# Kernel optimization log

Measured on AMD Instinct MI355X. Metric: run time of the kernel, lower is better.

The kernel has to match this reference:

```python
import jax, jax.numpy as jnp
import numpy as np

B, C, CO, N = 2, 32, 32, 64
MODES, LMAX, RBINS = 16, 2, 16
HALF = MODES // 2
NL = (LMAX + 1) ** 2  # 9 real spherical harmonics up to l=2
M = MODES ** 3
HID = 16  # round(CO * 0.5)


def _build_basis():
    # frequencies of the kept FNO corner modes along each axis
    f = np.concatenate([np.arange(HALF), np.arange(-HALF, 0)]).astype(np.float32)
    kx, ky, kz = np.meshgrid(f, f, f, indexing='ij')
    kx, ky, kz = kx.ravel(), ky.ravel(), kz.ravel()
    r = np.sqrt(kx ** 2 + ky ** 2 + kz ** 2)
    nzm = (r > 0).astype(np.float32)
    inv = np.where(r > 0, 1.0 / np.maximum(r, 1e-9), 0.0)
    ux, uy, uz = kx * inv, ky * inv, kz * inv
    # real spherical harmonics l=0,1,2 (cartesian form); all l>0 vanish at DC
    Y = np.stack([
        0.282095 * np.ones_like(r),
        0.488603 * uy, 0.488603 * uz, 0.488603 * ux,
        1.092548 * ux * uy, 1.092548 * uy * uz,
        0.315392 * (3.0 * uz ** 2 - nzm),
        1.092548 * ux * uz, 0.546274 * (ux ** 2 - uy ** 2)], axis=0)  # [NL, M]
    shell = np.minimum((r / (r.max() + 1e-6) * RBINS).astype(np.int64), RBINS - 1)
    cnt = np.bincount(shell, minlength=RBINS).astype(np.float32)
    w = 1.0 / np.sqrt(np.maximum(cnt, 1.0))
    mask = (shell[None, :] == np.arange(RBINS)[:, None]).astype(np.float32) * w[:, None]  # [RBINS, M]
    return (mask[:, None, :] * Y[None]).reshape(RBINS * NL, M).astype(np.float32)

BASIS = jnp.asarray(_build_basis())  # [K=144, M=4096], fixed projection basis
IDX = jnp.asarray(np.concatenate([np.arange(HALF), np.arange(N - HALF, N)]))  # kept mode indices


def cgelu(z):
    return jax.nn.gelu(z.real) + 1j * jax.nn.gelu(z.imag)


def setup_inputs() -> dict:
    key = jax.random.key(0)
    ks = jax.random.split(key, 17)
    rn = lambda k, s: jax.random.normal(k, s, dtype=jnp.float32)
    return {
        'x': rn(ks[0], (B, C, N, N, N)),
        'w_fno_r': rn(ks[1], (CO, C)) * 0.1, 'w_fno_i': rn(ks[2], (CO, C)) * 0.1,
        'b_fno_r': rn(ks[3], (CO,)) * 0.1, 'b_fno_i': rn(ks[4], (CO,)) * 0.1,
        'w_gate_r': rn(ks[5], (CO,)), 'w_gate_i': rn(ks[6], (CO,)),
        'w_spec_r': rn(ks[7], (RBINS, NL, C, CO)) * 0.1, 'w_spec_i': rn(ks[8], (RBINS, NL, C, CO)) * 0.1,
        'mlp_w1_r': rn(ks[9], (HID, CO)) * 0.1, 'mlp_w1_i': rn(ks[10], (HID, CO)) * 0.1,
        'mlp_b1_r': rn(ks[11], (HID,)) * 0.1, 'mlp_b1_i': rn(ks[12], (HID,)) * 0.1,
        'mlp_w2_r': rn(ks[13], (CO, HID)) * 0.1, 'mlp_w2_i': rn(ks[14], (CO, HID)) * 0.1,
        'mlp_b2_r': rn(ks[15], (CO,)) * 0.1, 'mlp_b2_i': rn(ks[16], (CO,)) * 0.1,
    }


def reference(x, w_fno_r, w_fno_i, b_fno_r, b_fno_i, w_gate_r, w_gate_i,
              w_spec_r, w_spec_i, mlp_w1_r, mlp_w1_i, mlp_b1_r, mlp_b1_i,
              mlp_w2_r, mlp_w2_i, mlp_b2_r, mlp_b2_i):
    cx = lambda r, i: (r + 1j * i).astype(jnp.complex64)
    xc = x.astype(jnp.complex64)
    w_fno, b_fno = cx(w_fno_r, w_fno_i), cx(b_fno_r, b_fno_i)
    w_gate = cx(w_gate_r, w_gate_i)
    w_spec = cx(w_spec_r, w_spec_i)
    w1, b1 = cx(mlp_w1_r, mlp_w1_i), cx(mlp_b1_r, mlp_b1_i)
    w2, b2 = cx(mlp_w2_r, mlp_w2_i), cx(mlp_b2_r, mlp_b2_i)

    # skip paths: complex 1x1-conv ('linear') and complex soft-gating
    skip_fno = jnp.einsum('oc,bcxyz->boxyz', w_fno, xc) + b_fno[None, :, None, None, None]
    skip_mlp = xc * w_gate[None, :, None, None, None]

    # Harmonic layer: FFT -> slice kept modes -> harmonic/radial projection
    # -> complex spectral conv -> inverse projection -> scatter -> iFFT
    xf = jnp.fft.fftn(xc, axes=(-3, -2, -1))
    xs = xf[:, :, IDX[:, None, None], IDX[None, :, None], IDX[None, None, :]].reshape(B, C, M)
    coeffs = jnp.einsum('bcm,km->bck', xs, BASIS).reshape(B, C, RBINS, NL)
    coeffs = jnp.einsum('bisl,slio->bosl', coeffs, w_spec)
    xs2 = jnp.einsum('bck,km->bcm', coeffs.reshape(B, CO, RBINS * NL), BASIS)
    full = jnp.zeros((B, CO, N, N, N), jnp.complex64).at[
        :, :, IDX[:, None, None], IDX[None, :, None], IDX[None, None, :]
    ].set(xs2.reshape(B, CO, MODES, MODES, MODES))
    x_fno = jnp.fft.ifftn(full, axes=(-3, -2, -1))

    x1 = x_fno + skip_fno  # n_layers=1 -> no activation here
    h = cgelu(jnp.einsum('hc,bcxyz->bhxyz', w1, x1) + b1[None, :, None, None, None])
    y = jnp.einsum('oh,bhxyz->boxyz', w2, h) + b2[None, :, None, None, None]
    return (y + skip_mlp).real
```

## Files before the change

kernel.cpp:

```cpp
#include <hip/hip_runtime.h>
#include <hip/hip_bf16.h>

#define PI2 6.283185307179586f

typedef __attribute__((ext_vector_type(8))) short short8;
typedef __attribute__((ext_vector_type(4))) float f32x4;

static const size_t O_Y      = 0;
static const size_t O_W1RT   = 36864;
static const size_t O_W1IT   = 37376;
static const size_t O_W1XR   = 37888;
static const size_t O_W1XI   = 38400;
static const size_t O_B1PR   = 38912;
static const size_t O_B1PI   = 38928;
static const size_t O_WSH    = 38944;
static const size_t O_SHELL  = 38960;
static const size_t O_ORDER  = 43056;
static const size_t O_SSTART = 47152;
static const size_t O_COEF   = 47232;
static const size_t O_COEF2  = 65664;
static const size_t O_XS     = 84096;
static const size_t O_XS2    = 608384;
static const size_t O_T2     = 1132672;
static const size_t O_T1     = 3229824;

static __device__ __forceinline__ float geluf(float v) {
  float u = 0.7978845608028654f * (v + 0.044715f * v * v * v);
  float a = fabsf(u);
  float e = __expf(-2.0f * a);
  float th = (1.0f - e) / (1.0f + e);
  th = copysignf(th, u);
  return 0.5f * v * (1.0f + th);
}

static __device__ __forceinline__ unsigned int f2bfbits(float f) {
  unsigned int u = __float_as_uint(f);
  u += 0x7fffu + ((u >> 16) & 1u);
  return u >> 16;
}

static __device__ __forceinline__ unsigned int pk2(float a, float b) {
  return f2bfbits(a) | (f2bfbits(b) << 16);
}

__global__ __launch_bounds__(256) void k0_init(
    const float* __restrict__ wfr, const float* __restrict__ wfi,
    const float* __restrict__ bfr, const float* __restrict__ bfi,
    const float* __restrict__ w1r, const float* __restrict__ w1i,
    const float* __restrict__ b1r, const float* __restrict__ b1i,
    float* __restrict__ ws) {
  float* Y    = ws + O_Y;
  float* w1rt = ws + O_W1RT;  float* w1it = ws + O_W1IT;
  float* W1xr = ws + O_W1XR;  float* W1xi = ws + O_W1XI;
  float* b1pr = ws + O_B1PR;  float* b1pi = ws + O_B1PI;
  float* wsh  = ws + O_WSH;
  int* shellOf = (int*)(ws + O_SHELL);
  int* order   = (int*)(ws + O_ORDER);
  int* sstart  = (int*)(ws + O_SSTART);

  __shared__ int cnt[16], fill[16], st[17];
  int tid = threadIdx.x;
  if (tid < 16) { cnt[tid] = 0; fill[tid] = 0; }
  __syncthreads();
  for (int m = tid; m < 4096; m += 256) {
    int ix = m >> 8, iy = (m >> 4) & 15, iz = m & 15;
    float kx = (float)(ix < 8 ? ix : ix - 16);
    float ky = (float)(iy < 8 ? iy : iy - 16);
    float kz = (float)(iz < 8 ? iz : iz - 16);
    float r2 = kx*kx + ky*ky + kz*kz;
    float r  = sqrtf(r2);
    float nzm = r2 > 0.f ? 1.f : 0.f;
    float inv = r2 > 0.f ? 1.0f / fmaxf(r, 1e-9f) : 0.f;
    float ux = kx*inv, uy = ky*inv, uz = kz*inv;
    Y[0*4096+m] = 0.282095f;
    Y[1*4096+m] = 0.488603f * uy;
    Y[2*4096+m] = 0.488603f * uz;
    Y[3*4096+m] = 0.488603f * ux;
    Y[4*4096+m] = 1.092548f * ux*uy;
    Y[5*4096+m] = 1.092548f * uy*uz;
    Y[6*4096+m] = 0.315392f * (3.0f*uz*uz - nzm);
    Y[7*4096+m] = 1.092548f * ux*uz;
    Y[8*4096+m] = 0.546274f * (ux*ux - uy*uy);
    float rmax = sqrtf(192.0f);
    float t = r / (rmax + 1e-6f) * 16.0f;
    int sh = (int)t; sh = sh > 15 ? 15 : sh;
    shellOf[m] = sh;
    atomicAdd(&cnt[sh], 1);
  }
  __syncthreads();
  if (tid == 0) { int a = 0; for (int s = 0; s < 16; ++s) { st[s] = a; a += cnt[s]; } st[16] = a; }
  __syncthreads();
  if (tid < 16) wsh[tid] = 1.0f / sqrtf(fmaxf((float)cnt[tid], 1.0f));
  if (tid < 17) sstart[tid] = st[tid];
  for (int m = tid; m < 4096; m += 256) {
    int sh = shellOf[m];
    int p = atomicAdd(&fill[sh], 1);
    order[st[sh] + p] = m;
  }
  for (int e = tid; e < 512; e += 256) {
    int j = e >> 5, c = e & 31;
    float ar = 0.f, ai = 0.f;
    for (int o = 0; o < 32; ++o) {
      float wr_ = w1r[j*32+o], wi_ = w1i[j*32+o];
      float fr  = wfr[o*32+c], fi_ = wfi[o*32+c];
      ar += wr_*fr - wi_*fi_;
      ai += wr_*fi_ + wi_*fr;
    }
    W1xr[c*16+j] = ar;  W1xi[c*16+j] = ai;
    w1rt[c*16+j] = w1r[j*32+c];
    w1it[c*16+j] = w1i[j*32+c];
  }
  if (tid < 16) {
    int j = tid;
    float ar = b1r[j], ai = b1i[j];
    for (int o = 0; o < 32; ++o) {
      ar += w1r[j*32+o]*bfr[o] - w1i[j*32+o]*bfi[o];
      ai += w1r[j*32+o]*bfi[o] + w1i[j*32+o]*bfr[o];
    }
    b1pr[j] = ar; b1pi[j] = ai;
  }
}

__global__ __launch_bounds__(256) void k12_fwd(const float* __restrict__ x, float* __restrict__ T2) {
  __shared__ float plane[64*68];
  __shared__ float2 slab[64*17];
  float* ysum = plane;
  float2* tw2 = (float2*)(plane + 2592);
  int blk = blockIdx.x;
  const float* src = x + (size_t)blk * 4096;
  int tid = threadIdx.x;
  for (int i = tid; i < 4096; i += 256) {
    int y = i >> 6, z = i & 63;
    plane[z*68 + y] = src[i];
  }
  __syncthreads();
  {
    int kz = tid & 15, yq = tid >> 4;
    float f = (float)(kz < 8 ? kz : kz - 16);
    float ang = -PI2 * f / 64.0f;
    float sw, cw; __sincosf(ang, &sw, &cw);
    float tr = 1.f, ti = 0.f;
    float a0r=0,a0i=0,a1r=0,a1i=0,a2r=0,a2i=0,a3r=0,a3i=0;
    for (int z = 0; z < 64; ++z) {
      float4 xv = *(const float4*)&plane[z*68 + 4*yq];
      a0r += xv.x*tr; a0i += xv.x*ti;
      a1r += xv.y*tr; a1i += xv.y*ti;
      a2r += xv.z*tr; a2i += xv.z*ti;
      a3r += xv.w*tr; a3i += xv.w*ti;
      float nt = tr*cw - ti*sw; ti = tr*sw + ti*cw; tr = nt;
    }
    int y0 = 4*yq;
    slab[(y0+0)*17 + kz] = make_float2(a0r, a0i);
    slab[(y0+1)*17 + kz] = make_float2(a1r, a1i);
    slab[(y0+2)*17 + kz] = make_float2(a2r, a2i);
    slab[(y0+3)*17 + kz] = make_float2(a3r, a3i);
  }
  __syncthreads();
  {
    int k = tid >> 4, i2 = tid & 15;
    float f = (float)(k < 8 ? k : k - 16);
    float ang = -PI2 * f * (float)i2 / 64.0f;
    float sw, cw; __sincosf(ang, &sw, &cw);
    tw2[k*17 + i2] = make_float2(cw, sw);
  }
  {
    int y0 = tid >> 4, kz = tid & 15;
    float2 u0 = slab[(y0     )*17 + kz];
    float2 u1 = slab[(y0 + 16)*17 + kz];
    float2 u2 = slab[(y0 + 32)*17 + kz];
    float2 u3 = slab[(y0 + 48)*17 + kz];
    float Ar = u0.x + u2.x, Ai = u0.y + u2.y;
    float Br = u0.x - u2.x, Bi = u0.y - u2.y;
    float Cr = u1.x + u3.x, Ci = u1.y + u3.y;
    float Dr = u1.x - u3.x, Di = u1.y - u3.y;
    float* yp = ysum + y0*162 + kz*10;
    yp[0] = Ar + Cr;  yp[1] = Ai + Ci;
    yp[2] = Br + Di;  yp[3] = Bi - Dr;
    yp[4] = Ar - Cr;  yp[5] = Ai - Ci;
    yp[6] = Br - Di;  yp[7] = Bi + Dr;
  }
  __syncthreads();
  {
    int kz = tid & 15, kyi = tid >> 4;
    const float* yp = ysum + kz*10 + (kyi & 3)*2;
    const float2* twp = tw2 + kyi*17;
    float ar = 0.f, ai = 0.f;
    #pragma unroll
    for (int y0 = 0; y0 < 16; ++y0) {
      float sr = yp[y0*162], si = yp[y0*162 + 1];
      float2 tw = twp[y0];
      ar += sr*tw.x - si*tw.y;
      ai += sr*tw.y + si*tw.x;
    }
    *(float2*)&T2[(size_t)blk*512 + (kyi*16 + kz)*2] = make_float2(ar, ai);
  }
}

__global__ __launch_bounds__(256) void k3_dftx(const float* __restrict__ T2, float* __restrict__ xs) {
  __shared__ float slab[64*34];
  __shared__ float xsum[2592];
  __shared__ float2 twx[16*17];
  int blk = blockIdx.x;
  int bc = blk >> 4, ky = blk & 15;
  int tid = threadIdx.x;
  for (int i = tid; i < 2048; i += 256) {
    int xr = i >> 5, rem = i & 31;
    slab[xr*34 + rem] = T2[((size_t)(bc*64 + xr)*16 + ky)*32 + rem];
  }
  {
    int k = tid >> 4, i2 = tid & 15;
    float f = (float)(k < 8 ? k : k - 16);
    float ang = -PI2 * f * (float)i2 / 64.0f;
    float sw, cw; __sincosf(ang, &sw, &cw);
    twx[k*17 + i2] = make_float2(cw, sw);
  }
  __syncthreads();
  {
    int x0 = tid >> 4, kz = tid & 15;
    const float2* sp = (const float2*)slab;
    float2 u0 = sp[(x0     )*17 + kz];
    float2 u1 = sp[(x0 + 16)*17 + kz];
    float2 u2 = sp[(x0 + 32)*17 + kz];
    float2 u3 = sp[(x0 + 48)*17 + kz];
    float Ar = u0.x + u2.x, Ai = u0.y + u2.y;
    float Br = u0.x - u2.x, Bi = u0.y - u2.y;
    float Cr = u1.x + u3.x, Ci = u1.y + u3.y;
    float Dr = u1.x - u3.x, Di = u1.y - u3.y;
    float* yp = xsum + x0*162 + kz*10;
    yp[0] = Ar + Cr;  yp[1] = Ai + Ci;
    yp[2] = Br + Di;  yp[3] = Bi - Dr;
    yp[4] = Ar - Cr;  yp[5] = Ai - Ci;
    yp[6] = Br - Di;  yp[7] = Bi + Dr;
  }
  __syncthreads();
  {
    int kz = tid & 15, kxi = tid >> 4;
    const float* yp = xsum + kz*10 + (kxi & 3)*2;
    const float2* twp = twx + kxi*17;
    float ar = 0.f, ai = 0.f;
    #pragma unroll
    for (int x0 = 0; x0 < 16; ++x0) {
      float sr = yp[x0*162], si = yp[x0*162 + 1];
      float2 tw = twp[x0];
      ar += sr*tw.x - si*tw.y;
      ai += sr*tw.y + si*tw.x;
    }
    *(float2*)&xs[(size_t)bc*8192 + (kxi*256 + ky*16 + kz)*2] = make_float2(ar, ai);
  }
}

__global__ __launch_bounds__(256) void k4_proj(const float* __restrict__ xs, const float* __restrict__ Y,
    const int* __restrict__ order, const int* __restrict__ sstart, const float* __restrict__ wsh,
    float* __restrict__ coeffs) {
  int blk = blockIdx.x; int bc = blk >> 4, s = blk & 15;
  int tid = threadIdx.x;
  int st = sstart[s], en = sstart[s+1];
  float ar[9], ai[9];
  #pragma unroll
  for (int l = 0; l < 9; ++l) { ar[l] = 0.f; ai[l] = 0.f; }
  for (int ii = st + tid; ii < en; ii += 256) {
    int m = order[ii];
    float2 v = *(const float2*)&xs[(size_t)bc*8192 + m*2];
    #pragma unroll
    for (int l = 0; l < 9; ++l) {
      float yv = Y[l*4096 + m];
      ar[l] += yv * v.x; ai[l] += yv * v.y;
    }
  }
  __shared__ float red[256*19];
  #pragma unroll
  for (int l = 0; l < 9; ++l) { red[tid*19 + l] = ar[l]; red[tid*19 + 9 + l] = ai[l]; }
  __syncthreads();
  for (int r = 128; r >= 1; r >>= 1) {
    if (tid < r) {
      #pragma unroll
      for (int q = 0; q < 18; ++q) red[tid*19 + q] += red[(tid + r)*19 + q];
    }
    __syncthreads();
  }
  if (tid == 0) {
    float w = wsh[s];
    for (int l = 0; l < 9; ++l) {
      coeffs[((size_t)bc*144 + s*9 + l)*2]     = w * red[l];
      coeffs[((size_t)bc*144 + s*9 + l)*2 + 1] = w * red[9 + l];
    }
  }
}

__global__ __launch_bounds__(64) void k5_spec(const float* __restrict__ coeffs,
    const float* __restrict__ wsr, const float* __restrict__ wsi, float* __restrict__ coeffs2) {
  int blk = blockIdx.x;
  int b = blk / 144, sl = blk % 144;
  int o = threadIdx.x;
  if (o >= 32) return;
  float ar = 0.f, ai = 0.f;
  for (int i = 0; i < 32; ++i) {
    float cr = coeffs[((size_t)(b*32 + i)*144 + sl)*2];
    float ci = coeffs[((size_t)(b*32 + i)*144 + sl)*2 + 1];
    float wr = wsr[(sl*32 + i)*32 + o];
    float wi = wsi[(sl*32 + i)*32 + o];
    ar += cr*wr - ci*wi;
    ai += cr*wi + ci*wr;
  }
  const float sc = 1.0f / 262144.0f;
  coeffs2[((size_t)(b*32 + o)*144 + sl)*2]     = ar * sc;
  coeffs2[((size_t)(b*32 + o)*144 + sl)*2 + 1] = ai * sc;
}

__global__ __launch_bounds__(256) void k7_unproj(const float* __restrict__ coeffs2, const float* __restrict__ Y,
    const int* __restrict__ shellOf, const float* __restrict__ wsh, float* __restrict__ xs2) {
  int bo = blockIdx.x >> 4;
  int m = ((blockIdx.x & 15) << 8) | threadIdx.x;
  __shared__ float c2[288];
  for (int i = threadIdx.x; i < 288; i += 256) c2[i] = coeffs2[(size_t)bo*288 + i];
  __syncthreads();
  int sh = shellOf[m];
  float w = wsh[sh];
  float ar = 0.f, ai = 0.f;
  #pragma unroll
  for (int l = 0; l < 9; ++l) {
    float yv = Y[l*4096 + m];
    ar += yv * c2[(sh*9 + l)*2];
    ai += yv * c2[(sh*9 + l)*2 + 1];
  }
  xs2[(size_t)bo*8192 + m*2]     = w * ar;
  xs2[(size_t)bo*8192 + m*2 + 1] = w * ai;
}

__global__ __launch_bounds__(256) void k8_invx(const float* __restrict__ xs2, float* __restrict__ U1) {
  __shared__ float slab[512];
  int blk = blockIdx.x;
  int bo = blk >> 4, ky = blk & 15;
  int tid = threadIdx.x;
  for (int i = tid; i < 512; i += 256) {
    int kx = i >> 5, rem = i & 31;
    slab[i] = xs2[(size_t)bo*8192 + kx*512 + ky*32 + rem];
  }
  __syncthreads();
  int kz = tid & 15, grp = tid >> 4;
  float ang = PI2 * (float)grp / 64.0f;
  float sw, cw; __sincosf(ang, &sw, &cw);
  float tr = 1.f, ti = 0.f;
  float sjr[4] = {0.f,0.f,0.f,0.f}, sji[4] = {0.f,0.f,0.f,0.f};
  #pragma unroll
  for (int kx = 0; kx < 16; ++kx) {
    if (kx == 8) ti = -ti;
    float2 v = *(const float2*)&slab[(kx*16 + kz)*2];
    sjr[kx & 3] += v.x*tr - v.y*ti;
    sji[kx & 3] += v.x*ti + v.y*tr;
    float nt = tr*cw - ti*sw; ti = tr*sw + ti*cw; tr = nt;
  }
  float Ar = sjr[0]+sjr[2], Ai = sji[0]+sji[2];
  float Br = sjr[0]-sjr[2], Bi = sji[0]-sji[2];
  float Cr = sjr[1]+sjr[3], Ci = sji[1]+sji[3];
  float Dr = sjr[1]-sjr[3], Di = sji[1]-sji[3];
  *(float2*)&U1[((size_t)(bo*64 + grp     )*16 + ky)*32 + kz*2] = make_float2(Ar+Cr, Ai+Ci);
  *(float2*)&U1[((size_t)(bo*64 + grp + 16)*16 + ky)*32 + kz*2] = make_float2(Br-Di, Bi+Dr);
  *(float2*)&U1[((size_t)(bo*64 + grp + 32)*16 + ky)*32 + kz*2] = make_float2(Ar-Cr, Ai-Ci);
  *(float2*)&U1[((size_t)(bo*64 + grp + 48)*16 + ky)*32 + kz*2] = make_float2(Br+Di, Bi-Dr);
}

__global__ __launch_bounds__(256) void k9_invy(const float* __restrict__ U1, float* __restrict__ U2) {
  __shared__ float slab[512];
  int blk = blockIdx.x;
  int tid = threadIdx.x;
  const float* src = U1 + (size_t)blk * 512;
  for (int i = tid; i < 512; i += 256) slab[i] = src[i];
  __syncthreads();
  int kz = tid & 15, grp = tid >> 4;
  float ang = PI2 * (float)grp / 64.0f;
  float sw, cw; __sincosf(ang, &sw, &cw);
  float tr = 1.f, ti = 0.f;
  float sjr[4] = {0.f,0.f,0.f,0.f}, sji[4] = {0.f,0.f,0.f,0.f};
  #pragma unroll
  for (int ky = 0; ky < 16; ++ky) {
    if (ky == 8) ti = -ti;
    float2 v = *(const float2*)&slab[(ky*16 + kz)*2];
    sjr[ky & 3] += v.x*tr - v.y*ti;
    sji[ky & 3] += v.x*ti + v.y*tr;
    float nt = tr*cw - ti*sw; ti = tr*sw + ti*cw; tr = nt;
  }
  float Ar = sjr[0]+sjr[2], Ai = sji[0]+sji[2];
  float Br = sjr[0]-sjr[2], Bi = sji[0]-sji[2];
  float Cr = sjr[1]+sjr[3], Ci = sji[1]+sji[3];
  float Dr = sjr[1]-sjr[3], Di = sji[1]-sji[3];
  float* dst = U2 + (size_t)blk * 2048;
  *(float2*)&dst[((grp     )*16 + kz)*2] = make_float2(Ar+Cr, Ai+Ci);
  *(float2*)&dst[((grp + 16)*16 + kz)*2] = make_float2(Br-Di, Bi+Dr);
  *(float2*)&dst[((grp + 32)*16 + kz)*2] = make_float2(Ar-Cr, Ai-Ci);
  *(float2*)&dst[((grp + 48)*16 + kz)*2] = make_float2(Br+Di, Bi-Dr);
}

__global__ __launch_bounds__(256) void k10_final(
    const float* __restrict__ x, const float* __restrict__ U2,
    const float* __restrict__ ws,
    const float* __restrict__ w2r, const float* __restrict__ w2i,
    const float* __restrict__ b2r, const float* __restrict__ wgr,
    float* __restrict__ out) {
  const float* w1rt = ws + O_W1RT;  const float* w1it = ws + O_W1IT;
  const float* W1xr = ws + O_W1XR;  const float* W1xi = ws + O_W1XI;
  const float* b1pr = ws + O_B1PR;  const float* b1pi = ws + O_B1PI;

  __shared__ unsigned int xfT[128*33];
  __shared__ __hip_bfloat16 xlT[128*34];
  __shared__ unsigned int hpW[4*272];
  float* scratch = (float*)xfT;
  float2* twz = (float2*)hpW;

  int tid = threadIdx.x;
  int blk = blockIdx.x;
  int yb = blk & 31, bx = blk >> 5;
  int b = bx >> 6, xr = bx & 63;
  int y0 = yb * 2;

  for (int i = tid; i < 1024; i += 256) {
    int ya = i >> 9, c = (i >> 4) & 31, zq = i & 15;
    const float4 v = *(const float4*)&x[(size_t)(b*32 + c)*262144 + (size_t)xr*4096
                                        + (size_t)(y0 + ya)*64 + 4*zq];
    int rb = ((ya << 6) + 4*zq)*34 + c;
    xlT[rb]       = __float2bfloat16(v.x);
    xlT[rb + 34]  = __float2bfloat16(v.y);
    xlT[rb + 68]  = __float2bfloat16(v.z);
    xlT[rb + 102] = __float2bfloat16(v.w);
  }
  for (int e = tid; e < 1024; e += 256) {
    int q = e & 15, o = (e >> 4) & 31, ya = e >> 9;
    const float2* g = (const float2*)(U2 + ((size_t)((b*32 + o)*64 + xr))*2048 + (size_t)(y0 + ya)*32);
    *(float2*)&scratch[(ya*32 + o)*34 + 2*q] = g[q];
  }
  {
    int k = tid >> 4, i2 = tid & 15;
    float f = (float)(k < 8 ? k : k - 16);
    float ang = PI2 * f * (float)i2 / 64.0f;
    float sw, cw; __sincosf(ang, &sw, &cw);
    twz[k*17 + i2] = make_float2(cw, sw);
  }
  __syncthreads();

  {
    int o = tid & 31, r3 = tid >> 5;
    int ya = r3 >> 2, zq = r3 & 3;
    float ur[16], ui[16];
    const float2* sp = (const float2*)&scratch[(ya*32 + o)*34];
    #pragma unroll
    for (int q = 0; q < 16; ++q) { float2 v = sp[q]; ur[q] = v.x; ui[q] = v.y; }
    __syncthreads();

    #pragma unroll
    for (int t = 0; t < 4; ++t) {
      int z0 = 4*zq + t;
      float sr[4] = {0.f, 0.f, 0.f, 0.f}, si[4] = {0.f, 0.f, 0.f, 0.f};
      #pragma unroll
      for (int k = 0; k < 16; ++k) {
        float2 tw = twz[k*17 + z0];
        sr[k & 3] += ur[k]*tw.x - ui[k]*tw.y;
        si[k & 3] += ur[k]*tw.y + ui[k]*tw.x;
      }
      float Ar = sr[0]+sr[2], Ai = si[0]+si[2];
      float Br = sr[0]-sr[2], Bi = si[0]-si[2];
      float Cr = sr[1]+sr[3], Ci = si[1]+si[3];
      float Dr = sr[1]-sr[3], Di = si[1]-si[3];
      int rb = (ya << 6) + z0;
      xfT[rb*33 + o]        = pk2(Ar+Cr, Ai+Ci);
      xfT[(rb+16)*33 + o]   = pk2(Br-Di, Bi+Dr);
      xfT[(rb+32)*33 + o]   = pk2(Ar-Cr, Ai-Ci);
      xfT[(rb+48)*33 + o]   = pk2(Br+Di, Bi-Dr);
    }
  }
  __syncthreads();

  {
    int lane = tid & 63, wv = tid >> 6;
    int p = lane & 15, q = lane >> 4;
    int wb = wv * 272;

    union U8 { short8 v; unsigned int u[4]; };
    U8 fW1r, fW1i, fW1iN, fW1xr, fW1xi, fW2[2];
    #pragma unroll
    for (int s = 0; s < 4; ++s) {
      int c0 = 8*q + 2*s, c1 = c0 + 1;
      fW1r.u[s]  = pk2(w1rt[c0*16 + p], w1rt[c1*16 + p]);
      fW1i.u[s]  = pk2(w1it[c0*16 + p], w1it[c1*16 + p]);
      fW1iN.u[s] = fW1i.u[s] ^ 0x80008000u;
      fW1xr.u[s] = pk2(W1xr[c0*16 + p], W1xr[c1*16 + p]);
      fW1xi.u[s] = pk2(W1xi[c0*16 + p], W1xi[c1*16 + p]);
    }
    #pragma unroll
    for (int mt = 0; mt < 2; ++mt) {
      int o = mt*16 + p;
      #pragma unroll
      for (int s = 0; s < 4; ++s) {
        int k0 = 8*q + 2*s;
        float a  = (k0   < 16) ? w2r[o*16 + k0]      : -w2i[o*16 + k0 - 16];
        float bb = (k0+1 < 16) ? w2r[o*16 + k0 + 1]  : -w2i[o*16 + k0 - 15];
        fW2[mt].u[s] = pk2(a, bb);
      }
    }
    float4 b1r4 = *(const float4*)(b1pr + 4*q);
    float4 b1i4 = *(const float4*)(b1pi + 4*q);
    float b2a[2][4], wga[2][4];
    #pragma unroll
    for (int mt = 0; mt < 2; ++mt) {
      float4 t0 = *(const float4*)(b2r + mt*16 + 4*q);
      float4 t1 = *(const float4*)(wgr + mt*16 + 4*q);
      b2a[mt][0]=t0.x; b2a[mt][1]=t0.y; b2a[mt][2]=t0.z; b2a[mt][3]=t0.w;
      wga[mt][0]=t1.x; wga[mt][1]=t1.y; wga[mt][2]=t1.z; wga[mt][3]=t1.w;
    }
    float b1ra[4] = {b1r4.x, b1r4.y, b1r4.z, b1r4.w};
    float b1ia[4] = {b1i4.x, b1i4.y, b1i4.z, b1i4.w};

    f32x4 zacc = {0.f, 0.f, 0.f, 0.f};
    const unsigned int* xlW = (const unsigned int*)xlT;

    for (int tt = 0; tt < 2; ++tt) {
      int tile = wv*2 + tt;
      int ya = tile >> 2, zg = tile & 3;
      int row = ya*64 + zg*16 + p;

      unsigned int w8[8];
      #pragma unroll
      for (int jj = 0; jj < 8; ++jj) w8[jj] = xfT[row*33 + 8*q + jj];
      U8 FR, FI, XV;
      #pragma unroll
      for (int s = 0; s < 4; ++s) {
        FR.u[s] = __builtin_amdgcn_perm(w8[2*s+1], w8[2*s], 0x05040100u);
        FI.u[s] = __builtin_amdgcn_perm(w8[2*s+1], w8[2*s], 0x07060302u);
        XV.u[s] = xlW[row*17 + 4*q + s];
      }

      f32x4 accR = zacc, accI = zacc;
      accR = __builtin_amdgcn_mfma_f32_16x16x32_bf16(fW1r.v,  FR.v, accR, 0, 0, 0);
      accR = __builtin_amdgcn_mfma_f32_16x16x32_bf16(fW1iN.v, FI.v, accR, 0, 0, 0);
      accR = __builtin_amdgcn_mfma_f32_16x16x32_bf16(fW1xr.v, XV.v, accR, 0, 0, 0);
      accI = __builtin_amdgcn_mfma_f32_16x16x32_bf16(fW1r.v,  FI.v, accI, 0, 0, 0);
      accI = __builtin_amdgcn_mfma_f32_16x16x32_bf16(fW1i.v,  FR.v, accI, 0, 0, 0);
      accI = __builtin_amdgcn_mfma_f32_16x16x32_bf16(fW1xi.v, XV.v, accI, 0, 0, 0);

      float hr_[4], hi_[4];
      #pragma unroll
      for (int r = 0; r < 4; ++r) {
        hr_[r] = geluf(accR[r] + b1ra[r]);
        hi_[r] = geluf(accI[r] + b1ia[r]);
      }
      hpW[wb + 17*p + 2*q]     = pk2(hr_[0], hr_[1]);
      hpW[wb + 17*p + 2*q + 1] = pk2(hr_[2], hr_[3]);
      hpW[wb + 17*p + 8 + 2*q]     = pk2(hi_[0], hi_[1]);
      hpW[wb + 17*p + 8 + 2*q + 1] = pk2(hi_[2], hi_[3]);

      U8 FH;
      #pragma unroll
      for (int s = 0; s < 4; ++s) FH.u[s] = hpW[wb + 17*p + 4*q + s];

      #pragma unroll
      for (int mt = 0; mt < 2; ++mt) {
        f32x4 accO = __builtin_amdgcn_mfma_f32_16x16x32_bf16(fW2[mt].v, FH.v, zacc, 0, 0, 0);
        #pragma unroll
        for (int r = 0; r < 4; ++r) {
          int o = mt*16 + q*4 + r;
          int z = zg*16 + p;
          float xv = __bfloat162float(xlT[row*34 + o]);
          out[(size_t)(b*32 + o)*262144 + (size_t)xr*4096 + (size_t)(y0 + ya)*64 + z]
              = accO[r] + b2a[mt][r] + wga[mt][r]*xv;
        }
      }
    }
  }
}

extern "C" void kernel_launch(void* const* d_in, const int* in_sizes, int n_in,
                              void* d_out, int out_size, void* d_ws, size_t ws_size,
                              hipStream_t stream) {
  (void)in_sizes; (void)n_in; (void)out_size; (void)ws_size;
  const float* x   = (const float*)d_in[0];
  const float* wfr = (const float*)d_in[1];
  const float* wfi = (const float*)d_in[2];
  const float* bfr = (const float*)d_in[3];
  const float* bfi = (const float*)d_in[4];
  const float* wgr = (const float*)d_in[5];
  const float* wsr = (const float*)d_in[7];
  const float* wsi = (const float*)d_in[8];
  const float* w1r = (const float*)d_in[9];
  const float* w1i = (const float*)d_in[10];
  const float* b1r = (const float*)d_in[11];
  const float* b1i = (const float*)d_in[12];
  const float* w2r = (const float*)d_in[13];
  const float* w2i = (const float*)d_in[14];
  const float* b2r = (const float*)d_in[15];
  float* out = (float*)d_out;
  float* ws  = (float*)d_ws;

  float* T1      = ws + O_T1;
  float* T2      = ws + O_T2;
  float* xs      = ws + O_XS;
  float* xs2     = ws + O_XS2;
  float* coeffs  = ws + O_COEF;
  float* coeffs2 = ws + O_COEF2;
  float* Y       = ws + O_Y;
  int* shellOf   = (int*)(ws + O_SHELL);
  int* order     = (int*)(ws + O_ORDER);
  int* sstart    = (int*)(ws + O_SSTART);
  float* wsh     = ws + O_WSH;

  hipLaunchKernelGGL(k0_init,  dim3(1),    dim3(256), 0, stream, wfr, wfi, bfr, bfi, w1r, w1i, b1r, b1i, ws);
  hipLaunchKernelGGL(k12_fwd,  dim3(4096), dim3(256), 0, stream, x, T2);
  hipLaunchKernelGGL(k3_dftx,  dim3(1024), dim3(256), 0, stream, T2, xs);
  hipLaunchKernelGGL(k4_proj,  dim3(1024), dim3(256), 0, stream, xs, Y, order, sstart, wsh, coeffs);
  hipLaunchKernelGGL(k5_spec,  dim3(288),  dim3(64),  0, stream, coeffs, wsr, wsi, coeffs2);
  hipLaunchKernelGGL(k7_unproj,dim3(1024), dim3(256), 0, stream, coeffs2, Y, shellOf, wsh, xs2);
  hipLaunchKernelGGL(k8_invx,  dim3(1024), dim3(256), 0, stream, xs2, T2);
  hipLaunchKernelGGL(k9_invy,  dim3(4096), dim3(256), 0, stream, T2, T1);
  hipLaunchKernelGGL(k10_final,dim3(4096), dim3(256), 0, stream, x, T1, ws, w2r, w2i, b2r, wgr, out);
}
```

Baseline: 273.9 us.

## Radix-4 pre-split z DFT in forward kernel and vectorize twiddle loads

```diff
diff --git a/kernel.cpp b/kernel.cpp
--- a/kernel.cpp
+++ b/kernel.cpp
@@ -122,47 +122,82 @@
 }
 
 __global__ __launch_bounds__(256) void k12_fwd(const float* __restrict__ x, float* __restrict__ T2) {
-  __shared__ float plane[64*68];
+  __shared__ __align__(16) float zS[4096];
   __shared__ float2 slab[64*17];
-  float* ysum = plane;
-  float2* tw2 = (float2*)(plane + 2592);
+  __shared__ float2 tw[16*17];
+  float* zP = zS;  float* zQ = zS + 1024;  float* zB = zS + 2048;  float* zD = zS + 3072;
+  float* ysum = zS;
   int blk = blockIdx.x;
   const float* src = x + (size_t)blk * 4096;
   int tid = threadIdx.x;
-  for (int i = tid; i < 4096; i += 256) {
-    int y = i >> 6, z = i & 63;
-    plane[z*68 + y] = src[i];
-  }
-  __syncthreads();
-  {
-    int kz = tid & 15, yq = tid >> 4;
-    float f = (float)(kz < 8 ? kz : kz - 16);
-    float ang = -PI2 * f / 64.0f;
-    float sw, cw; __sincosf(ang, &sw, &cw);
-    float tr = 1.f, ti = 0.f;
-    float a0r=0,a0i=0,a1r=0,a1i=0,a2r=0,a2i=0,a3r=0,a3i=0;
-    for (int z = 0; z < 64; ++z) {
-      float4 xv = *(const float4*)&plane[z*68 + 4*yq];
-      a0r += xv.x*tr; a0i += xv.x*ti;
-      a1r += xv.y*tr; a1i += xv.y*ti;
-      a2r += xv.z*tr; a2i += xv.z*ti;
-      a3r += xv.w*tr; a3i += xv.w*ti;
-      float nt = tr*cw - ti*sw; ti = tr*sw + ti*cw; tr = nt;
-    }
-    int y0 = 4*yq;
-    slab[(y0+0)*17 + kz] = make_float2(a0r, a0i);
-    slab[(y0+1)*17 + kz] = make_float2(a1r, a1i);
-    slab[(y0+2)*17 + kz] = make_float2(a2r, a2i);
-    slab[(y0+3)*17 + kz] = make_float2(a3r, a3i);
-  }
-  __syncthreads();
+
+  {
+    int y = tid >> 2, zt = tid & 3;
+    const float4* s4 = (const float4*)(src + y*64);
+    float4 u0 = s4[zt];
+    float4 u1 = s4[zt + 4];
+    float4 u2 = s4[zt + 8];
+    float4 u3 = s4[zt + 12];
+    const float* p0 = (const float*)&u0; const float* p1 = (const float*)&u1;
+    const float* p2 = (const float*)&u2; const float* p3 = (const float*)&u3;
+    int base = 4*zt*64 + y;
+    #pragma unroll
+    for (int e = 0; e < 4; ++e) {
+      float a = p0[e] + p2[e], c = p1[e] + p3[e];
+      float bb = p0[e] - p2[e], d = p1[e] - p3[e];
+      zP[base + e*64] = a + c;
+      zQ[base + e*64] = a - c;
+      zB[base + e*64] = bb;
+      zD[base + e*64] = d;
+    }
+  }
   {
     int k = tid >> 4, i2 = tid & 15;
     float f = (float)(k < 8 ? k : k - 16);
     float ang = -PI2 * f * (float)i2 / 64.0f;
     float sw, cw; __sincosf(ang, &sw, &cw);
-    tw2[k*17 + i2] = make_float2(cw, sw);
-  }
+    tw[k*17 + i2] = make_float2(cw, sw);
+  }
+  __syncthreads();
+
+  {
+    int kz = tid & 15, yq = tid >> 4;
+    int j = kz & 3;
+    const float2* twp = tw + kz*17;
+    float arr[4] = {0.f,0.f,0.f,0.f}, aii[4] = {0.f,0.f,0.f,0.f};
+    if ((j & 1) == 0) {
+      const float* plane = (j == 0) ? zP : zQ;
+      #pragma unroll
+      for (int z0 = 0; z0 < 16; ++z0) {
+        float2 w = twp[z0];
+        float4 s = *(const float4*)&plane[z0*64 + 4*yq];
+        arr[0] += s.x*w.x; aii[0] += s.x*w.y;
+        arr[1] += s.y*w.x; aii[1] += s.y*w.y;
+        arr[2] += s.z*w.x; aii[2] += s.z*w.y;
+        arr[3] += s.w*w.x; aii[3] += s.w*w.y;
+      }
+    } else {
+      float dsg = (j == 1) ? -1.f : 1.f;
+      #pragma unroll
+      for (int z0 = 0; z0 < 16; ++z0) {
+        float2 w = twp[z0];
+        float4 b = *(const float4*)&zB[z0*64 + 4*yq];
+        float4 d = *(const float4*)&zD[z0*64 + 4*yq];
+        float swi = dsg * w.y, swr = dsg * w.x;
+        arr[0] += b.x*w.x - d.x*swi;  aii[0] += b.x*w.y + d.x*swr;
+        arr[1] += b.y*w.x - d.y*swi;  aii[1] += b.y*w.y + d.y*swr;
+        arr[2] += b.z*w.x - d.z*swi;  aii[2] += b.z*w.y + d.z*swr;
+        arr[3] += b.w*w.x - d.w*swi;  aii[3] += b.w*w.y + d.w*swr;
+      }
+    }
+    int y0 = 4*yq;
+    slab[(y0+0)*17 + kz] = make_float2(arr[0], aii[0]);
+    slab[(y0+1)*17 + kz] = make_float2(arr[1], aii[1]);
+    slab[(y0+2)*17 + kz] = make_float2(arr[2], aii[2]);
+    slab[(y0+3)*17 + kz] = make_float2(arr[3], aii[3]);
+  }
+  __syncthreads();
+
   {
     int y0 = tid >> 4, kz = tid & 15;
     float2 u0 = slab[(y0     )*17 + kz];
@@ -180,17 +215,18 @@
     yp[6] = Br - Di;  yp[7] = Bi + Dr;
   }
   __syncthreads();
+
   {
     int kz = tid & 15, kyi = tid >> 4;
     const float* yp = ysum + kz*10 + (kyi & 3)*2;
-    const float2* twp = tw2 + kyi*17;
+    const float2* twp = tw + kyi*17;
     float ar = 0.f, ai = 0.f;
     #pragma unroll
     for (int y0 = 0; y0 < 16; ++y0) {
       float sr = yp[y0*162], si = yp[y0*162 + 1];
-      float2 tw = twp[y0];
-      ar += sr*tw.x - si*tw.y;
-      ai += sr*tw.y + si*tw.x;
+      float2 w = twp[y0];
+      ar += sr*w.x - si*w.y;
+      ai += sr*w.y + si*w.x;
     }
     *(float2*)&T2[(size_t)blk*512 + (kyi*16 + kz)*2] = make_float2(ar, ai);
   }
@@ -241,9 +277,9 @@
     #pragma unroll
     for (int x0 = 0; x0 < 16; ++x0) {
       float sr = yp[x0*162], si = yp[x0*162 + 1];
-      float2 tw = twp[x0];
-      ar += sr*tw.x - si*tw.y;
-      ai += sr*tw.y + si*tw.x;
+      float2 w = twp[x0];
+      ar += sr*w.x - si*w.y;
+      ai += sr*w.y + si*w.x;
     }
     *(float2*)&xs[(size_t)bc*8192 + (kxi*256 + ky*16 + kz)*2] = make_float2(ar, ai);
   }
@@ -403,9 +439,9 @@
 
   __shared__ unsigned int xfT[128*33];
   __shared__ __hip_bfloat16 xlT[128*34];
-  __shared__ unsigned int hpW[4*272];
+  __shared__ f32x4 hpW4[272];
+  unsigned int* hpW = (unsigned int*)hpW4;
   float* scratch = (float*)xfT;
-  float2* twz = (float2*)hpW;
 
   int tid = threadIdx.x;
   int blk = blockIdx.x;
@@ -428,12 +464,15 @@
     const float2* g = (const float2*)(U2 + ((size_t)((b*32 + o)*64 + xr))*2048 + (size_t)(y0 + ya)*32);
     *(float2*)&scratch[(ya*32 + o)*34 + 2*q] = g[q];
   }
-  {
-    int k = tid >> 4, i2 = tid & 15;
-    float f = (float)(k < 8 ? k : k - 16);
-    float ang = PI2 * f * (float)i2 / 64.0f;
-    float sw, cw; __sincosf(ang, &sw, &cw);
-    twz[k*17 + i2] = make_float2(cw, sw);
+  if (tid < 128) {
+    int k2 = tid >> 4, i2 = tid & 15;
+    int ka = 2*k2, kb = ka + 1;
+    float f0 = (float)(ka < 8 ? ka : ka - 16);
+    float f1 = (float)(kb < 8 ? kb : kb - 16);
+    float s0, c0, s1, c1;
+    __sincosf(PI2 * f0 * (float)i2 / 64.0f, &s0, &c0);
+    __sincosf(PI2 * f1 * (float)i2 / 64.0f, &s1, &c1);
+    hpW4[k2*17 + i2] = (f32x4){c0, s0, c1, s1};
   }
   __syncthreads();
 
@@ -446,15 +485,19 @@
     for (int q = 0; q < 16; ++q) { float2 v = sp[q]; ur[q] = v.x; ui[q] = v.y; }
     __syncthreads();
 
+    const f32x4* twz4 = (const f32x4*)hpW4;
     #pragma unroll
     for (int t = 0; t < 4; ++t) {
       int z0 = 4*zq + t;
       float sr[4] = {0.f, 0.f, 0.f, 0.f}, si[4] = {0.f, 0.f, 0.f, 0.f};
       #pragma unroll
-      for (int k = 0; k < 16; ++k) {
-        float2 tw = twz[k*17 + z0];
-        sr[k & 3] += ur[k]*tw.x - ui[k]*tw.y;
-        si[k & 3] += ur[k]*tw.y + ui[k]*tw.x;
+      for (int k2 = 0; k2 < 8; ++k2) {
+        f32x4 w = twz4[k2*17 + z0];
+        int ka = 2*k2, kb = ka + 1;
+        sr[ka & 3] += ur[ka]*w[0] - ui[ka]*w[1];
+        si[ka & 3] += ur[ka]*w[1] + ui[ka]*w[0];
+        sr[kb & 3] += ur[kb]*w[2] - ui[kb]*w[3];
+        si[kb & 3] += ur[kb]*w[3] + ui[kb]*w[2];
       }
       float Ar = sr[0]+sr[2], Ai = si[0]+si[2];
       float Br = sr[0]-sr[2], Bi = si[0]-si[2];
```

Measured after the change: 269.2 us. Within noise of the previous version (-1.7%).
